# Performance work log

Measured on AMD Instinct MI355X. Metric: run time of the kernel, lower is better.

The kernel has to match this reference:

```python
import jax, jax.numpy as jnp
import numpy as np

WIN = 8
SHIFT = 4
HEADS = 6

def _rel_pos_index(w):
    coords = np.stack(np.meshgrid(np.arange(w), np.arange(w), indexing='ij'))  # (2,w,w)
    cf = coords.reshape(2, -1)
    rel = (cf[:, :, None] - cf[:, None, :]).transpose(1, 2, 0)  # (N,N,2)
    rel[:, :, 0] += w - 1
    rel[:, :, 1] += w - 1
    rel[:, :, 0] *= 2 * w - 1
    return rel.sum(-1)  # (N,N) int

def _attn_mask(H, W, w, s):
    img = np.zeros((H, W))
    slices = (slice(0, -w), slice(-w, -s), slice(-s, None))
    cnt = 0
    for hs in slices:
        for ws in slices:
            img[hs, ws] = cnt
            cnt += 1
    mw = img.reshape(H // w, w, W // w, w).transpose(0, 2, 1, 3).reshape(-1, w * w)  # (nW,N)
    am = mw[:, None, :] - mw[:, :, None]
    return np.where(am != 0, -100.0, 0.0).astype(np.float32)  # (nW,N,N)

def _ln(z, g, b):
    mu = z.mean(-1, keepdims=True)
    var = z.var(-1, keepdims=True)
    return (z - mu) / jnp.sqrt(var + 1e-5) * g + b

def setup_inputs() -> dict:
    key = jax.random.key(0)
    ks = jax.random.split(key, 8)
    C, HID = 192, 768
    sc = lambda fan: 1.0 / np.sqrt(fan)
    return {
        'x': jax.random.normal(ks[0], (4, 256, 256, C), jnp.float32),
        'qkv_w': jax.random.normal(ks[1], (3 * C, C), jnp.float32) * sc(C),
        'qkv_b': jnp.zeros((3 * C,), jnp.float32),
        'proj_w': jax.random.normal(ks[2], (C, C), jnp.float32) * sc(C),
        'proj_b': jnp.zeros((C,), jnp.float32),
        'rpb': jax.random.normal(ks[3], (225, HEADS), jnp.float32) * 0.02,
        'n1_w': jnp.ones((C,), jnp.float32),
        'n1_b': jnp.zeros((C,), jnp.float32),
        'n2_w': jnp.ones((C,), jnp.float32),
        'n2_b': jnp.zeros((C,), jnp.float32),
        'fc1_w': jax.random.normal(ks[4], (HID, C), jnp.float32) * sc(C),
        'fc1_b': jnp.zeros((HID,), jnp.float32),
        'fc2_w': jax.random.normal(ks[5], (C, HID), jnp.float32) * sc(HID),
        'fc2_b': jnp.zeros((C,), jnp.float32),
    }

def reference(x, qkv_w, qkv_b, proj_w, proj_b, rpb, n1_w, n1_b, n2_w, n2_b, fc1_w, fc1_b, fc2_w, fc2_b):
    B, H, W, C = x.shape
    N = WIN * WIN
    hd = C // HEADS
    scale = hd ** -0.5

    shortcut = x.reshape(B, H * W, C)
    z = _ln(shortcut, n1_w, n1_b).reshape(B, H, W, C)
    z = jnp.roll(z, (-SHIFT, -SHIFT), axis=(1, 2))

    # window partition -> (B*nW, N, C)
    xw = z.reshape(B, H // WIN, WIN, W // WIN, WIN, C).transpose(0, 1, 3, 2, 4, 5).reshape(-1, N, C)
    B_ = xw.shape[0]

    qkv = (xw @ qkv_w.T + qkv_b).reshape(B_, N, 3, HEADS, hd).transpose(2, 0, 3, 1, 4)
    q, k, v = qkv[0] * scale, qkv[1], qkv[2]
    attn = jnp.einsum('bhnd,bhmd->bhnm', q, k)  # (B_,H,N,N)

    idx = _rel_pos_index(WIN)
    bias = rpb[idx.reshape(-1)].reshape(N, N, HEADS).transpose(2, 0, 1)  # (H,N,N)
    attn = attn + bias[None]

    mask = jnp.asarray(_attn_mask(H, W, WIN, SHIFT))  # (nW,N,N)
    nW = mask.shape[0]
    attn = attn.reshape(B_ // nW, nW, HEADS, N, N) + mask[None, :, None]
    attn = jax.nn.softmax(attn, axis=-1).reshape(B_, HEADS, N, N)

    out = jnp.einsum('bhnm,bhmd->bhnd', attn, v).transpose(0, 2, 1, 3).reshape(B_, N, C)
    out = out @ proj_w.T + proj_b

    # window reverse
    out = out.reshape(B, H // WIN, W // WIN, WIN, WIN, C).transpose(0, 1, 3, 2, 4, 5).reshape(B, H, W, C)
    out = jnp.roll(out, (SHIFT, SHIFT), axis=(1, 2)).reshape(B, H * W, C)

    h = shortcut + out
    m = _ln(h, n2_w, n2_b)
    m = jax.nn.gelu(m @ fc1_w.T + fc1_b, approximate=False)
    m = m @ fc2_w.T + fc2_b
    return (h + m).reshape(B, H, W, C)
```

## Files before the change

kernel.cpp:

```cpp
#include <hip/hip_runtime.h>
#include <hip/hip_bf16.h>

typedef __attribute__((ext_vector_type(8))) __bf16 bf16x8;
typedef __attribute__((ext_vector_type(4))) float f32x4;
typedef __hip_bfloat16 bf16;

#define SCALE_Q 0.17677669529663687f

#define LDSP(p) ((__attribute__((address_space(3))) unsigned int*)(unsigned long long)(p))
#define GPTR(p) ((const __attribute__((address_space(1))) unsigned int*)(unsigned long long)(p))
#define GLD16(gp, lp) __builtin_amdgcn_global_load_lds(GPTR(gp), LDSP(lp), 16, 0, 0)

__device__ inline float gelu_f(float x) {
  const float ax = fabsf(x) * 0.70710678118654752f;
  const float t = __builtin_amdgcn_rcpf(__builtin_fmaf(0.3275911f, ax, 1.0f));
  const float poly = t * __builtin_fmaf(t, __builtin_fmaf(t, __builtin_fmaf(t,
                     __builtin_fmaf(t, 1.061405429f, -1.453152027f),
                     1.421413741f), -0.284496736f), 0.254829592f);
  const float er = __builtin_fmaf(-poly, __expf(-ax * ax), 1.0f);
  return 0.5f * x * (1.0f + copysignf(er, x));
}

__global__ void cvt_kernel(const float* __restrict__ in, bf16* __restrict__ out, int n) {
  int i = blockIdx.x * 256 + threadIdx.x;
  if (i < n) out[i] = __float2bfloat16(in[i]);
}

template<int K, int KC>
__global__ void cvt_frag_kernel(const float* __restrict__ in, bf16* __restrict__ out, int total) {
  int i = blockIdx.x * 256 + threadIdx.x;
  if (i < total) {
    const int n = i / K, k = i - n * K;
    out[((n >> 4) * KC + (k >> 5)) * 512 + ((k >> 3) & 3) * 128 + (n & 15) * 8 + (k & 7)] =
        __float2bfloat16(in[i]);
  }
}

__global__ __launch_bounds__(256) void ln_kernel(const float* __restrict__ in,
                                                 const float* __restrict__ gw,
                                                 const float* __restrict__ gb,
                                                 bf16* __restrict__ out) {
  const int t = blockIdx.x * 4 + (threadIdx.x >> 6);
  const int lane = threadIdx.x & 63;
  const int b_ = t >> 6, n = t & 63;
  const int b = b_ >> 10, wk = b_ & 1023, wi = wk >> 5, wj = wk & 31;
  const int i_ = n >> 3, j_ = n & 7;
  const int hf = (wi * 8 + i_ + 4) & 255, wf = (wj * 8 + j_ + 4) & 255;
  const long g = (((long)b * 256 + hf) * 256 + wf) * 192;
  const float x0 = in[g + lane], x1 = in[g + 64 + lane], x2 = in[g + 128 + lane];
  float s = x0 + x1 + x2;
  float s2 = x0 * x0 + x1 * x1 + x2 * x2;
  #pragma unroll
  for (int m = 1; m < 64; m <<= 1) { s += __shfl_xor(s, m); s2 += __shfl_xor(s2, m); }
  const float mu = s * (1.0f / 192.0f);
  const float rstd = rsqrtf(s2 * (1.0f / 192.0f) - mu * mu + 1e-5f);
  const long o = (long)t * 192;
  out[o + lane]       = __float2bfloat16((x0 - mu) * rstd * gw[lane]       + gb[lane]);
  out[o + 64 + lane]  = __float2bfloat16((x1 - mu) * rstd * gw[lane + 64]  + gb[lane + 64]);
  out[o + 128 + lane] = __float2bfloat16((x2 - mu) * rstd * gw[lane + 128] + gb[lane + 128]);
}

template<int EPI>
__global__ __launch_bounds__(512, 4) void gemm_bt(const bf16* __restrict__ A,
                                                  const bf16* __restrict__ Bw,
                                                  const float* __restrict__ bias,
                                                  int K, void* __restrict__ outp,
                                                  const float* __restrict__ aux1,
                                                  const float* __restrict__ aux2) {
  __shared__ __align__(16) bf16 Ald[128 * 64];
  __shared__ __align__(16) bf16 Bld[192 * 64];
  const int tid = threadIdx.x;
  const int n0 = blockIdx.x * 192;
  const long m0 = (long)blockIdx.y * 128;
  const int lane = tid & 63, wid = tid >> 6;
  const int wr = (wid >> 1) * 32, wc = (wid & 1) * 96;
  const int lg = lane >> 4, lr = lane & 15;
  const int l3 = lane >> 3, l7 = lane & 7;
  const int chunk = l7 ^ l3;

  const bf16* aptr = A + (m0 + wid * 16 + l3) * (long)K + chunk * 8;
  const bf16* bptr = Bw + (n0 + wid * 24 + l3) * (long)K + chunk * 8;
  char* alds = (char*)Ald + wid * 16 * 128;
  char* blds = (char*)Bld + wid * 24 * 128;
  const long rk8 = 8 * (long)K;

  f32x4 acc[2][6];
  #pragma unroll
  for (int i = 0; i < 2; i++)
    #pragma unroll
    for (int j = 0; j < 6; j++) acc[i][j] = (f32x4){0.f, 0.f, 0.f, 0.f};

  for (int k0 = 0; k0 < K; k0 += 64) {
    GLD16(aptr + k0, alds);
    GLD16(aptr + rk8 + k0, alds + 1024);
    GLD16(bptr + k0, blds);
    GLD16(bptr + rk8 + k0, blds + 1024);
    GLD16(bptr + 2 * rk8 + k0, blds + 2048);
    __syncthreads();
    #pragma unroll
    for (int ks = 0; ks < 2; ks++) {
      bf16x8 af[2], bfr[6];
      #pragma unroll
      for (int i = 0; i < 2; i++) {
        const int row = wr + i * 16 + lr;
        af[i] = *(const bf16x8*)((const char*)Ald + row * 128 + (((ks * 4 + lg) ^ (row & 7)) * 16));
      }
      #pragma unroll
      for (int j = 0; j < 6; j++) {
        const int row = wc + j * 16 + lr;
        bfr[j] = *(const bf16x8*)((const char*)Bld + row * 128 + (((ks * 4 + lg) ^ (row & 7)) * 16));
      }
      #pragma unroll
      for (int i = 0; i < 2; i++)
        #pragma unroll
        for (int j = 0; j < 6; j++)
          acc[i][j] = __builtin_amdgcn_mfma_f32_16x16x32_bf16(af[i], bfr[j], acc[i][j], 0, 0, 0);
    }
    __syncthreads();
  }

  #pragma unroll
  for (int i = 0; i < 2; i++) {
    #pragma unroll
    for (int j = 0; j < 6; j++) {
      #pragma unroll
      for (int r = 0; r < 4; r++) {
        const long m = m0 + wr + i * 16 + lg * 4 + r;
        const int cn = n0 + wc + j * 16 + lr;
        float v = acc[i][j][r] + bias[cn];
        if (EPI == 0) {
          const long b_ = m >> 6; const int n = (int)(m & 63);
          const int which = cn / 192, rem = cn - which * 192, head = rem >> 5, d = rem & 31;
          if (which == 0) v *= SCALE_Q;
          ((bf16*)outp)[((b_ * 6 + head) * 3 + which) * 2048 + n * 32 + d] = __float2bfloat16(v);
        } else {
          const long b_ = m >> 6; const int n = (int)(m & 63);
          const int b = (int)(b_ >> 10), wk = (int)(b_ & 1023), wi = wk >> 5, wj = wk & 31;
          const int i_ = n >> 3, j_ = n & 7;
          const int hf = (wi * 8 + i_ + 4) & 255, wf = (wj * 8 + j_ + 4) & 255;
          const long g = (((long)b * 256 + hf) * 256 + wf) * 192 + cn;
          ((float*)outp)[g] = aux1[g] + v;
        }
      }
    }
  }
}

__global__ __launch_bounds__(512, 2) void mlp_fused(const float* __restrict__ hbuf,
                                                    const float* __restrict__ n2w,
                                                    const float* __restrict__ n2b,
                                                    const bf16* __restrict__ w1t,
                                                    const float* __restrict__ b1,
                                                    const bf16* __restrict__ w2t,
                                                    const float* __restrict__ b2,
                                                    float* __restrict__ outp) {
  __shared__ __align__(16) char smem[122880];
  char* Ab = smem;
  char* G  = smem + 24576;

  const int tid = threadIdx.x;
  const long m0 = (long)blockIdx.x * 64;
  const int lane = tid & 63, wid = tid >> 6;
  const int lg = lane >> 4, lr = lane & 15;

  #pragma unroll
  for (int t8 = 0; t8 < 8; t8++) {
    const int row = wid * 8 + t8;
    const long g = (m0 + row) * 192;
    const float x0 = hbuf[g + lane], x1 = hbuf[g + 64 + lane], x2 = hbuf[g + 128 + lane];
    float s = x0 + x1 + x2;
    float s2 = x0 * x0 + x1 * x1 + x2 * x2;
    #pragma unroll
    for (int msk = 1; msk < 64; msk <<= 1) { s += __shfl_xor(s, msk); s2 += __shfl_xor(s2, msk); }
    const float mu = s * (1.0f / 192.0f);
    const float rstd = rsqrtf(s2 * (1.0f / 192.0f) - mu * mu + 1e-5f);
    #pragma unroll
    for (int p = 0; p < 3; p++) {
      const int ch = p * 64 + lane;
      const float xv = (p == 0) ? x0 : (p == 1) ? x1 : x2;
      const float v = (xv - mu) * rstd * n2w[ch] + n2b[ch];
      const int c = (ch >> 3) & 7;
      const int slot = c ^ (row & 7);
      *(unsigned short*)(Ab + p * 8192 + row * 128 + slot * 16 + (ch & 7) * 2) =
          __builtin_bit_cast(unsigned short, __float2bfloat16(v));
    }
  }
  __syncthreads();

  f32x4 acc1[4][6];
  #pragma unroll
  for (int i = 0; i < 4; i++)
    #pragma unroll
    for (int j = 0; j < 6; j++) acc1[i][j] = (f32x4){0.f, 0.f, 0.f, 0.f};

  const int c16base = wid * 6;
  #pragma unroll
  for (int kc = 0; kc < 6; kc++) {
    const int q = kc >> 1;
    const int kk = (kc & 1) * 4 + lg;
    bf16x8 af[4], bfr[6];
    #pragma unroll
    for (int i = 0; i < 4; i++) {
      const int row = i * 16 + lr;
      af[i] = *(const bf16x8*)(Ab + q * 8192 + row * 128 + ((kk ^ (row & 7)) * 16));
    }
    #pragma unroll
    for (int j = 0; j < 6; j++)
      bfr[j] = *(const bf16x8*)(w1t + ((c16base + j) * 6 + kc) * 512 + lane * 8);
    #pragma unroll
    for (int i = 0; i < 4; i++)
      #pragma unroll
      for (int j = 0; j < 6; j++)
        acc1[i][j] = __builtin_amdgcn_mfma_f32_16x16x32_bf16(af[i], bfr[j], acc1[i][j], 0, 0, 0);
  }

  #pragma unroll
  for (int j = 0; j < 6; j++) {
    const int n = wid * 96 + j * 16 + lr;
    const float bj = b1[n];
    const int c = n >> 3;
    #pragma unroll
    for (int i = 0; i < 4; i++) {
      #pragma unroll
      for (int r = 0; r < 4; r++) {
        const int m = i * 16 + lg * 4 + r;
        const int slot = (c & ~7) | ((c & 7) ^ (m & 7));
        *(unsigned short*)(G + m * 1536 + slot * 16 + (n & 7) * 2) =
            __builtin_bit_cast(unsigned short, __float2bfloat16(gelu_f(acc1[i][j][r] + bj)));
      }
    }
  }
  __syncthreads();

  const int wt = wid >> 2, wn = wid & 3;
  f32x4 acc2[2][3];
  #pragma unroll
  for (int i = 0; i < 2; i++)
    #pragma unroll
    for (int j = 0; j < 3; j++) acc2[i][j] = (f32x4){0.f, 0.f, 0.f, 0.f};

  for (int kt = 0; kt < 24; kt++) {
    const int c2 = kt * 4 + lg;
    bf16x8 af2[2], bfr2[3];
    #pragma unroll
    for (int i = 0; i < 2; i++) {
      const int grow = wt * 32 + i * 16 + lr;
      const int slot2 = (c2 & ~7) | ((c2 & 7) ^ (grow & 7));
      af2[i] = *(const bf16x8*)(G + grow * 1536 + slot2 * 16);
    }
    #pragma unroll
    for (int j = 0; j < 3; j++)
      bfr2[j] = *(const bf16x8*)(w2t + ((wn * 3 + j) * 24 + kt) * 512 + lane * 8);
    #pragma unroll
    for (int i = 0; i < 2; i++)
      #pragma unroll
      for (int j = 0; j < 3; j++)
        acc2[i][j] = __builtin_amdgcn_mfma_f32_16x16x32_bf16(af2[i], bfr2[j], acc2[i][j], 0, 0, 0);
  }

  #pragma unroll
  for (int j = 0; j < 3; j++) {
    const int cn = wn * 48 + j * 16 + lr;
    const float bj = b2[cn];
    #pragma unroll
    for (int i = 0; i < 2; i++) {
      #pragma unroll
      for (int r = 0; r < 4; r++) {
        const long m = m0 + wt * 32 + i * 16 + lg * 4 + r;
        outp[m * 192 + cn] = acc2[i][j][r] + bj + hbuf[m * 192 + cn];
      }
    }
  }
}

__global__ __launch_bounds__(64) void attn_kernel(const bf16* __restrict__ qkv,
                                                  const float* __restrict__ rpb,
                                                  bf16* __restrict__ outp) {
  __shared__ __align__(16) char smem[14848];
  __shared__ float rps[225];
  const int bid = blockIdx.x;
  const int b_ = bid / 6, head = bid - b_ * 6;
  const int lane = threadIdx.x;
  const long base = ((long)b_ * 6 + head) * 3 * 2048;

  for (int t = lane; t < 225; t += 64) rps[t] = rpb[t * 6 + head];

  #pragma unroll
  for (int q = 0; q < 4; q++) {
    const int f = q * 64 + lane, row = f >> 2, c = f & 3;
    *(uint4*)(smem + row * 80 + c * 16) = *(const uint4*)(qkv + base + row * 32 + c * 8);
    *(uint4*)(smem + 5120 + row * 80 + c * 16) = *(const uint4*)(qkv + base + 2048 + row * 32 + c * 8);
  }
  {
    const bf16* vsrc = qkv + base + 4096 + lane * 32;
    bf16 vv[32];
    #pragma unroll
    for (int q = 0; q < 4; q++) *(uint4*)&vv[q * 8] = *(const uint4*)(vsrc + q * 8);
    bf16* vt = (bf16*)(smem + 10240);
    #pragma unroll
    for (int d = 0; d < 32; d++) vt[d * 72 + lane] = vv[d];
  }
  __syncthreads();

  const int lg = lane >> 4, lr = lane & 15;
  const f32x4 z4 = {0.f, 0.f, 0.f, 0.f};
  f32x4 s[4][4];
  {
    bf16x8 a[4], b[4];
    #pragma unroll
    for (int fi = 0; fi < 4; fi++)
      a[fi] = *(const bf16x8*)(smem + (fi * 16 + lr) * 80 + lg * 16);
    #pragma unroll
    for (int fj = 0; fj < 4; fj++)
      b[fj] = *(const bf16x8*)(smem + 5120 + (fj * 16 + lr) * 80 + lg * 16);
    #pragma unroll
    for (int fi = 0; fi < 4; fi++)
      #pragma unroll
      for (int fj = 0; fj < 4; fj++)
        s[fi][fj] = __builtin_amdgcn_mfma_f32_16x16x32_bf16(a[fi], b[fj], z4, 0, 0, 0);
  }

  const int wk = b_ & 1023; const int wi = wk >> 5, wj = wk & 31;
  const bool eh = (wi == 31), ew = (wj == 31);
  bf16* P = (bf16*)smem;
  #pragma unroll
  for (int fi = 0; fi < 4; fi++) {
    #pragma unroll
    for (int r = 0; r < 4; r++) {
      const int n = fi * 16 + lg * 4 + r;
      const int i1 = n >> 3, j1 = n & 7;
      const int labn = (eh ? (i1 < 4 ? 3 : 6) : 0) + (ew ? (j1 < 4 ? 1 : 2) : 0);
      float vals[4];
      #pragma unroll
      for (int fj = 0; fj < 4; fj++) {
        const int m = fj * 16 + lr;
        const int i2 = m >> 3, j2 = m & 7;
        const int labm = (eh ? (i2 < 4 ? 3 : 6) : 0) + (ew ? (j2 < 4 ? 1 : 2) : 0);
        vals[fj] = s[fi][fj][r] + rps[(i1 - i2 + 7) * 15 + (j1 - j2 + 7)]
                 + (labn != labm ? -100.0f : 0.0f);
      }
      float mx = fmaxf(fmaxf(vals[0], vals[1]), fmaxf(vals[2], vals[3]));
      #pragma unroll
      for (int msk = 1; msk < 16; msk <<= 1) mx = fmaxf(mx, __shfl_xor(mx, msk));
      float pe[4]; float sum = 0.f;
      #pragma unroll
      for (int fj = 0; fj < 4; fj++) { pe[fj] = __expf(vals[fj] - mx); sum += pe[fj]; }
      #pragma unroll
      for (int msk = 1; msk < 16; msk <<= 1) sum += __shfl_xor(sum, msk);
      const float rinv = 1.0f / sum;
      #pragma unroll
      for (int fj = 0; fj < 4; fj++)
        P[n * 72 + fj * 16 + lr] = __float2bfloat16(pe[fj] * rinv);
    }
  }
  __syncthreads();

  f32x4 o[4][2];
  #pragma unroll
  for (int fi = 0; fi < 4; fi++)
    #pragma unroll
    for (int fd = 0; fd < 2; fd++) o[fi][fd] = z4;
  const bf16* vt = (const bf16*)(smem + 10240);
  #pragma unroll
  for (int ks = 0; ks < 2; ks++) {
    bf16x8 pa[4], vb[2];
    #pragma unroll
    for (int fi = 0; fi < 4; fi++)
      pa[fi] = *(const bf16x8*)(P + (fi * 16 + lr) * 72 + ks * 32 + lg * 8);
    #pragma unroll
    for (int fd = 0; fd < 2; fd++)
      vb[fd] = *(const bf16x8*)(vt + (fd * 16 + lr) * 72 + ks * 32 + lg * 8);
    #pragma unroll
    for (int fi = 0; fi < 4; fi++)
      #pragma unroll
      for (int fd = 0; fd < 2; fd++)
        o[fi][fd] = __builtin_amdgcn_mfma_f32_16x16x32_bf16(pa[fi], vb[fd], o[fi][fd], 0, 0, 0);
  }
  #pragma unroll
  for (int fi = 0; fi < 4; fi++)
    #pragma unroll
    for (int fd = 0; fd < 2; fd++)
      #pragma unroll
      for (int r = 0; r < 4; r++) {
        const int n = fi * 16 + lg * 4 + r;
        outp[((long)b_ * 64 + n) * 192 + head * 32 + fd * 16 + lr] = __float2bfloat16(o[fi][fd][r]);
      }
}

extern "C" void kernel_launch(void* const* d_in, const int* in_sizes, int n_in,
                              void* d_out, int out_size, void* d_ws, size_t ws_size,
                              hipStream_t stream) {
  const float* x      = (const float*)d_in[0];
  const float* qkv_w  = (const float*)d_in[1];
  const float* qkv_b  = (const float*)d_in[2];
  const float* proj_w = (const float*)d_in[3];
  const float* proj_b = (const float*)d_in[4];
  const float* rpb    = (const float*)d_in[5];
  const float* n1_w   = (const float*)d_in[6];
  const float* n1_b   = (const float*)d_in[7];
  const float* n2_w   = (const float*)d_in[8];
  const float* n2_b   = (const float*)d_in[9];
  const float* fc1_w  = (const float*)d_in[10];
  const float* fc1_b  = (const float*)d_in[11];
  const float* fc2_w  = (const float*)d_in[12];
  const float* fc2_b  = (const float*)d_in[13];

  char* ws = (char*)d_ws;
  bf16* qkvw_h  = (bf16*)(ws);
  bf16* projw_h = (bf16*)(ws + 221184);
  bf16* fc1w_t  = (bf16*)(ws + 294912);
  bf16* fc2w_t  = (bf16*)(ws + 589824);
  bf16* r1      = (bf16*)(ws + (1L << 20));
  bf16* r2      = (bf16*)(ws + 101711872L);
  float* hbuf   = (float*)(ws + 504365056L);

  cvt_kernel<<<432, 256, 0, stream>>>(qkv_w, qkvw_h, 110592);
  cvt_kernel<<<144, 256, 0, stream>>>(proj_w, projw_h, 36864);
  cvt_frag_kernel<192, 6><<<576, 256, 0, stream>>>(fc1_w, fc1w_t, 147456);
  cvt_frag_kernel<768, 24><<<576, 256, 0, stream>>>(fc2_w, fc2w_t, 147456);

  ln_kernel<<<65536, 256, 0, stream>>>(x, n1_w, n1_b, r1);
  gemm_bt<0><<<dim3(3, 2048), 512, 0, stream>>>(r1, qkvw_h, qkv_b, 192, r2, nullptr, nullptr);
  attn_kernel<<<24576, 64, 0, stream>>>(r2, rpb, r1);
  gemm_bt<1><<<dim3(1, 2048), 512, 0, stream>>>(r1, projw_h, proj_b, 192, hbuf, x, nullptr);
  mlp_fused<<<4096, 512, 0, stream>>>(hbuf, n2_w, n2_b, fc1w_t, fc1_b, fc2w_t, fc2_b,
                                      (float*)d_out);
}
```

Baseline: 804.4 us.

## Load QKV/proj weights as pre-fragmented MFMA tiles directly from global memory

The QKV and projection weights are now converted into an MFMA fragment-ordered layout, so each lane reads its B operand with one contiguous 16-byte global load instead of staging B through LDS. The A tile for the whole K=192 is loaded into LDS once up front, which removes the per-K-step barriers and the loop. This cuts LDS traffic and synchronisation in the two small-K GEMMs. In exchange, B reads now come from L2/global with no LDS reuse, and the larger LDS footprint may lower occupancy.

```diff
diff --git a/kernel.cpp b/kernel.cpp
--- a/kernel.cpp
+++ b/kernel.cpp
@@ -19,11 +19,6 @@
                      1.421413741f), -0.284496736f), 0.254829592f);
   const float er = __builtin_fmaf(-poly, __expf(-ax * ax), 1.0f);
   return 0.5f * x * (1.0f + copysignf(er, x));
-}
-
-__global__ void cvt_kernel(const float* __restrict__ in, bf16* __restrict__ out, int n) {
-  int i = blockIdx.x * 256 + threadIdx.x;
-  if (i < n) out[i] = __float2bfloat16(in[i]);
 }
 
 template<int K, int KC>
@@ -61,14 +56,12 @@
 }
 
 template<int EPI>
-__global__ __launch_bounds__(512, 4) void gemm_bt(const bf16* __restrict__ A,
-                                                  const bf16* __restrict__ Bw,
-                                                  const float* __restrict__ bias,
-                                                  int K, void* __restrict__ outp,
-                                                  const float* __restrict__ aux1,
-                                                  const float* __restrict__ aux2) {
-  __shared__ __align__(16) bf16 Ald[128 * 64];
-  __shared__ __align__(16) bf16 Bld[192 * 64];
+__global__ __launch_bounds__(512, 4) void gemm_fragB(const bf16* __restrict__ A,
+                                                     const bf16* __restrict__ Bwt,
+                                                     const float* __restrict__ bias,
+                                                     void* __restrict__ outp,
+                                                     const float* __restrict__ aux1) {
+  __shared__ __align__(16) char Ab[49152];
   const int tid = threadIdx.x;
   const int n0 = blockIdx.x * 192;
   const long m0 = (long)blockIdx.y * 128;
@@ -78,11 +71,16 @@
   const int l3 = lane >> 3, l7 = lane & 7;
   const int chunk = l7 ^ l3;
 
-  const bf16* aptr = A + (m0 + wid * 16 + l3) * (long)K + chunk * 8;
-  const bf16* bptr = Bw + (n0 + wid * 24 + l3) * (long)K + chunk * 8;
-  char* alds = (char*)Ald + wid * 16 * 128;
-  char* blds = (char*)Bld + wid * 24 * 128;
-  const long rk8 = 8 * (long)K;
+  {
+    const bf16* aptr = A + (m0 + wid * 16 + l3) * 192 + chunk * 8;
+    char* alds = Ab + wid * 2048;
+    #pragma unroll
+    for (int q = 0; q < 3; q++) {
+      GLD16(aptr + q * 64, alds + q * 16384);
+      GLD16(aptr + 8 * 192 + q * 64, alds + q * 16384 + 1024);
+    }
+  }
+  __syncthreads();
 
   f32x4 acc[2][6];
   #pragma unroll
@@ -90,33 +88,25 @@
     #pragma unroll
     for (int j = 0; j < 6; j++) acc[i][j] = (f32x4){0.f, 0.f, 0.f, 0.f};
 
-  for (int k0 = 0; k0 < K; k0 += 64) {
-    GLD16(aptr + k0, alds);
-    GLD16(aptr + rk8 + k0, alds + 1024);
-    GLD16(bptr + k0, blds);
-    GLD16(bptr + rk8 + k0, blds + 1024);
-    GLD16(bptr + 2 * rk8 + k0, blds + 2048);
-    __syncthreads();
-    #pragma unroll
-    for (int ks = 0; ks < 2; ks++) {
-      bf16x8 af[2], bfr[6];
-      #pragma unroll
-      for (int i = 0; i < 2; i++) {
-        const int row = wr + i * 16 + lr;
-        af[i] = *(const bf16x8*)((const char*)Ald + row * 128 + (((ks * 4 + lg) ^ (row & 7)) * 16));
-      }
-      #pragma unroll
-      for (int j = 0; j < 6; j++) {
-        const int row = wc + j * 16 + lr;
-        bfr[j] = *(const bf16x8*)((const char*)Bld + row * 128 + (((ks * 4 + lg) ^ (row & 7)) * 16));
-      }
-      #pragma unroll
-      for (int i = 0; i < 2; i++)
-        #pragma unroll
-        for (int j = 0; j < 6; j++)
-          acc[i][j] = __builtin_amdgcn_mfma_f32_16x16x32_bf16(af[i], bfr[j], acc[i][j], 0, 0, 0);
-    }
-    __syncthreads();
+  const int c16base = (n0 >> 4) + (wid & 1) * 6;
+  #pragma unroll
+  for (int kc = 0; kc < 6; kc++) {
+    const int q = kc >> 1;
+    const int kk = (kc & 1) * 4 + lg;
+    bf16x8 af[2], bfr[6];
+    #pragma unroll
+    for (int i = 0; i < 2; i++) {
+      const int row = wr + i * 16 + lr;
+      af[i] = *(const bf16x8*)(Ab + q * 16384 + row * 128 + ((kk ^ (row & 7)) * 16));
+    }
+    #pragma unroll
+    for (int j = 0; j < 6; j++)
+      bfr[j] = *(const bf16x8*)(Bwt + ((c16base + j) * 6 + kc) * 512 + lane * 8);
+    #pragma unroll
+    for (int i = 0; i < 2; i++)
+      #pragma unroll
+      for (int j = 0; j < 6; j++)
+        acc[i][j] = __builtin_amdgcn_mfma_f32_16x16x32_bf16(af[i], bfr[j], acc[i][j], 0, 0, 0);
   }
 
   #pragma unroll
@@ -406,23 +396,23 @@
   const float* fc2_b  = (const float*)d_in[13];
 
   char* ws = (char*)d_ws;
-  bf16* qkvw_h  = (bf16*)(ws);
-  bf16* projw_h = (bf16*)(ws + 221184);
+  bf16* qkvw_t  = (bf16*)(ws);
+  bf16* projw_t = (bf16*)(ws + 221184);
   bf16* fc1w_t  = (bf16*)(ws + 294912);
   bf16* fc2w_t  = (bf16*)(ws + 589824);
   bf16* r1      = (bf16*)(ws + (1L << 20));
   bf16* r2      = (bf16*)(ws + 101711872L);
   float* hbuf   = (float*)(ws + 504365056L);
 
-  cvt_kernel<<<432, 256, 0, stream>>>(qkv_w, qkvw_h, 110592);
-  cvt_kernel<<<144, 256, 0, stream>>>(proj_w, projw_h, 36864);
+  cvt_frag_kernel<192, 6><<<432, 256, 0, stream>>>(qkv_w, qkvw_t, 110592);
+  cvt_frag_kernel<192, 6><<<144, 256, 0, stream>>>(proj_w, projw_t, 36864);
   cvt_frag_kernel<192, 6><<<576, 256, 0, stream>>>(fc1_w, fc1w_t, 147456);
   cvt_frag_kernel<768, 24><<<576, 256, 0, stream>>>(fc2_w, fc2w_t, 147456);
 
   ln_kernel<<<65536, 256, 0, stream>>>(x, n1_w, n1_b, r1);
-  gemm_bt<0><<<dim3(3, 2048), 512, 0, stream>>>(r1, qkvw_h, qkv_b, 192, r2, nullptr, nullptr);
+  gemm_fragB<0><<<dim3(3, 2048), 512, 0, stream>>>(r1, qkvw_t, qkv_b, r2, nullptr);
   attn_kernel<<<24576, 64, 0, stream>>>(r2, rpb, r1);
-  gemm_bt<1><<<dim3(1, 2048), 512, 0, stream>>>(r1, projw_h, proj_b, 192, hbuf, x, nullptr);
+  gemm_fragB<1><<<dim3(1, 2048), 512, 0, stream>>>(r1, projw_t, proj_b, hbuf, x);
   mlp_fused<<<4096, 512, 0, stream>>>(hbuf, n2_w, n2_b, fc1w_t, fc1_b, fc2w_t, fc2_b,
                                       (float*)d_out);
 }
```

New measurement: 828.8 us. 1.03x slower.

## Fuse LayerNorm1 with QKV projection into a single kernel

Applied to the files above, without the earlier changes.

Replaces the standalone LN1 kernel and the QKV GEMM with one kernel. Each 64-row block normalizes shifted-window tokens into swizzled LDS as bf16, then runs MFMA against QKV weights pre-laid in fragment order, read straight from global memory. This removes the round trip of the normalized activations through HBM and one launch. The cost is that B fragments are re-read from global or L2 per block with no LDS staging, plus scattered 2-byte epilogue stores.

```diff
diff --git a/kernel.cpp b/kernel.cpp
--- a/kernel.cpp
+++ b/kernel.cpp
@@ -36,28 +36,91 @@
   }
 }
 
-__global__ __launch_bounds__(256) void ln_kernel(const float* __restrict__ in,
-                                                 const float* __restrict__ gw,
-                                                 const float* __restrict__ gb,
-                                                 bf16* __restrict__ out) {
-  const int t = blockIdx.x * 4 + (threadIdx.x >> 6);
-  const int lane = threadIdx.x & 63;
-  const int b_ = t >> 6, n = t & 63;
-  const int b = b_ >> 10, wk = b_ & 1023, wi = wk >> 5, wj = wk & 31;
-  const int i_ = n >> 3, j_ = n & 7;
-  const int hf = (wi * 8 + i_ + 4) & 255, wf = (wj * 8 + j_ + 4) & 255;
-  const long g = (((long)b * 256 + hf) * 256 + wf) * 192;
-  const float x0 = in[g + lane], x1 = in[g + 64 + lane], x2 = in[g + 128 + lane];
-  float s = x0 + x1 + x2;
-  float s2 = x0 * x0 + x1 * x1 + x2 * x2;
-  #pragma unroll
-  for (int m = 1; m < 64; m <<= 1) { s += __shfl_xor(s, m); s2 += __shfl_xor(s2, m); }
-  const float mu = s * (1.0f / 192.0f);
-  const float rstd = rsqrtf(s2 * (1.0f / 192.0f) - mu * mu + 1e-5f);
-  const long o = (long)t * 192;
-  out[o + lane]       = __float2bfloat16((x0 - mu) * rstd * gw[lane]       + gb[lane]);
-  out[o + 64 + lane]  = __float2bfloat16((x1 - mu) * rstd * gw[lane + 64]  + gb[lane + 64]);
-  out[o + 128 + lane] = __float2bfloat16((x2 - mu) * rstd * gw[lane + 128] + gb[lane + 128]);
+__global__ __launch_bounds__(512, 2) void qkv_ln1(const float* __restrict__ x,
+                                                  const float* __restrict__ n1w,
+                                                  const float* __restrict__ n1b,
+                                                  const bf16* __restrict__ qwt,
+                                                  const float* __restrict__ qb,
+                                                  bf16* __restrict__ outp) {
+  __shared__ __align__(16) char Ab[24576];
+  const int tid = threadIdx.x;
+  const long m0 = (long)blockIdx.x * 64;
+  const int lane = tid & 63, wid = tid >> 6;
+  const int lg = lane >> 4, lr = lane & 15;
+
+  #pragma unroll
+  for (int t8 = 0; t8 < 8; t8++) {
+    const int row = wid * 8 + t8;
+    const long t = m0 + row;
+    const int b_ = (int)(t >> 6), n = (int)(t & 63);
+    const int b = b_ >> 10, wk = b_ & 1023, wi = wk >> 5, wj = wk & 31;
+    const int hf = (wi * 8 + (n >> 3) + 4) & 255, wf = (wj * 8 + (n & 7) + 4) & 255;
+    const long g = (((long)b * 256 + hf) * 256 + wf) * 192;
+    const float x0 = x[g + lane], x1 = x[g + 64 + lane], x2 = x[g + 128 + lane];
+    float s = x0 + x1 + x2;
+    float s2 = x0 * x0 + x1 * x1 + x2 * x2;
+    #pragma unroll
+    for (int msk = 1; msk < 64; msk <<= 1) { s += __shfl_xor(s, msk); s2 += __shfl_xor(s2, msk); }
+    const float mu = s * (1.0f / 192.0f);
+    const float rstd = rsqrtf(s2 * (1.0f / 192.0f) - mu * mu + 1e-5f);
+    #pragma unroll
+    for (int p = 0; p < 3; p++) {
+      const int ch = p * 64 + lane;
+      const float xv = (p == 0) ? x0 : (p == 1) ? x1 : x2;
+      const float v = (xv - mu) * rstd * n1w[ch] + n1b[ch];
+      const int c = (ch >> 3) & 7;
+      const int slot = c ^ (row & 7);
+      *(unsigned short*)(Ab + p * 8192 + row * 128 + slot * 16 + (ch & 7) * 2) =
+          __builtin_bit_cast(unsigned short, __float2bfloat16(v));
+    }
+  }
+  __syncthreads();
+
+  const int wrr = (wid >> 2) * 32;
+  const int wcg = wid & 3;
+  f32x4 acc[2][9];
+  #pragma unroll
+  for (int i = 0; i < 2; i++)
+    #pragma unroll
+    for (int j = 0; j < 9; j++) acc[i][j] = (f32x4){0.f, 0.f, 0.f, 0.f};
+
+  const int c16base = wcg * 9;
+  #pragma unroll
+  for (int kc = 0; kc < 6; kc++) {
+    const int q = kc >> 1;
+    const int kk = (kc & 1) * 4 + lg;
+    bf16x8 af[2], bfr[9];
+    #pragma unroll
+    for (int i = 0; i < 2; i++) {
+      const int row = wrr + i * 16 + lr;
+      af[i] = *(const bf16x8*)(Ab + q * 8192 + row * 128 + ((kk ^ (row & 7)) * 16));
+    }
+    #pragma unroll
+    for (int j = 0; j < 9; j++)
+      bfr[j] = *(const bf16x8*)(qwt + ((c16base + j) * 6 + kc) * 512 + lane * 8);
+    #pragma unroll
+    for (int i = 0; i < 2; i++)
+      #pragma unroll
+      for (int j = 0; j < 9; j++)
+        acc[i][j] = __builtin_amdgcn_mfma_f32_16x16x32_bf16(af[i], bfr[j], acc[i][j], 0, 0, 0);
+  }
+
+  #pragma unroll
+  for (int i = 0; i < 2; i++) {
+    #pragma unroll
+    for (int j = 0; j < 9; j++) {
+      #pragma unroll
+      for (int r = 0; r < 4; r++) {
+        const long m = m0 + wrr + i * 16 + lg * 4 + r;
+        const int cn = wcg * 144 + j * 16 + lr;
+        float v = acc[i][j][r] + qb[cn];
+        const long b_ = m >> 6; const int n = (int)(m & 63);
+        const int which = cn / 192, rem = cn - which * 192, head = rem >> 5, d = rem & 31;
+        if (which == 0) v *= SCALE_Q;
+        outp[((b_ * 6 + head) * 3 + which) * 2048 + n * 32 + d] = __float2bfloat16(v);
+      }
+    }
+  }
 }
 
 template<int EPI>
@@ -406,7 +469,7 @@
   const float* fc2_b  = (const float*)d_in[13];
 
   char* ws = (char*)d_ws;
-  bf16* qkvw_h  = (bf16*)(ws);
+  bf16* qkvw_t  = (bf16*)(ws);
   bf16* projw_h = (bf16*)(ws + 221184);
   bf16* fc1w_t  = (bf16*)(ws + 294912);
   bf16* fc2w_t  = (bf16*)(ws + 589824);
@@ -414,13 +477,12 @@
   bf16* r2      = (bf16*)(ws + 101711872L);
   float* hbuf   = (float*)(ws + 504365056L);
 
-  cvt_kernel<<<432, 256, 0, stream>>>(qkv_w, qkvw_h, 110592);
+  cvt_frag_kernel<192, 6><<<432, 256, 0, stream>>>(qkv_w, qkvw_t, 110592);
   cvt_kernel<<<144, 256, 0, stream>>>(proj_w, projw_h, 36864);
   cvt_frag_kernel<192, 6><<<576, 256, 0, stream>>>(fc1_w, fc1w_t, 147456);
   cvt_frag_kernel<768, 24><<<576, 256, 0, stream>>>(fc2_w, fc2w_t, 147456);
 
-  ln_kernel<<<65536, 256, 0, stream>>>(x, n1_w, n1_b, r1);
-  gemm_bt<0><<<dim3(3, 2048), 512, 0, stream>>>(r1, qkvw_h, qkv_b, 192, r2, nullptr, nullptr);
+  qkv_ln1<<<4096, 512, 0, stream>>>(x, n1_w, n1_b, qkvw_t, qkv_b, r2);
   attn_kernel<<<24576, 64, 0, stream>>>(r2, rpb, r1);
   gemm_bt<1><<<dim3(1, 2048), 512, 0, stream>>>(r1, projw_h, proj_b, 192, hbuf, x, nullptr);
   mlp_fused<<<4096, 512, 0, stream>>>(hbuf, n2_w, n2_b, fc1w_t, fc1_b, fc2w_t, fc2_b,
```

New measurement: 803.8 us. No clear change (-0.1%).
